# Kernel optimization log

Measured on AMD Instinct MI355X. Metric: run time of the kernel, lower is better.

Reference implementation:

```python
import jax, jax.numpy as jnp
import numpy as np

N_NODES = 100000
N_EDGES = 400000
D = 128
BN_EPS = 1e-5


def setup_inputs() -> dict:
    key = jax.random.key(0)
    ks = jax.random.split(key, 8)
    lim = 1.0 / np.sqrt(D)  # torch Linear default init range
    feature = jax.random.normal(ks[0], (N_NODES, D), dtype=jnp.float32)
    edge_index = jax.random.randint(ks[1], (2, N_EDGES), 0, N_NODES, dtype=jnp.int64)
    w1 = jax.random.uniform(ks[2], (D, D), jnp.float32, -lim, lim)
    b1 = jax.random.uniform(ks[3], (D,), jnp.float32, -lim, lim)
    w2 = jax.random.uniform(ks[4], (D, D), jnp.float32, -lim, lim)
    b2 = jax.random.uniform(ks[5], (D,), jnp.float32, -lim, lim)
    gamma = jnp.ones((D,), jnp.float32)
    beta = jnp.zeros((D,), jnp.float32)
    return {"feature": feature, "edge_index": edge_index, "w1": w1, "b1": b1,
            "w2": w2, "b2": b2, "gamma": gamma, "beta": beta}


def reference(feature, edge_index, w1, b1, w2, b2, gamma, beta):
    n = feature.shape[0]
    src, dst = edge_index[0], edge_index[1]
    # GIN aggregation (eps=0): h_i = x_i + sum_{j: (j->i)} x_j
    agg = jax.ops.segment_sum(feature[src], dst, num_segments=n)
    h = feature + agg
    # 2-layer MLP: Linear -> ReLU -> Linear (torch Linear: x @ W.T + b)
    h = jnp.maximum(h @ w1.T + b1, 0.0) @ w2.T + b2
    # ReLU then BatchNorm1d (training mode: batch stats, biased variance)
    h = jnp.maximum(h, 0.0)
    mean = jnp.mean(h, axis=0)
    var = jnp.mean(jnp.square(h - mean), axis=0)
    return (h - mean) * jax.lax.rsqrt(var + BN_EPS) * gamma + beta
```

## Files before the change

kernel.cpp:

```cpp
#include <hip/hip_runtime.h>
#include <hip/hip_bf16.h>

#define DD 128
#define TM 64
#define LD 136
#define SB 128
#define GRID_MLP 1024

typedef short bf16x8 __attribute__((ext_vector_type(8)));
typedef float f32x4  __attribute__((ext_vector_type(4)));

__device__ __forceinline__ unsigned short f2bf(float f) {
  unsigned int u = __float_as_uint(f);
  u += 0x7FFFu + ((u >> 16) & 1u);
  return (unsigned short)(u >> 16);
}
__device__ __forceinline__ unsigned int pack2(float lo, float hi) {
  return (unsigned int)f2bf(lo) | ((unsigned int)f2bf(hi) << 16);
}
__device__ __forceinline__ float bf2f(unsigned short u) {
  union { unsigned int i; float f; } x; x.i = ((unsigned int)u) << 16; return x.f;
}
__device__ __forceinline__ void add2(float* a, unsigned int w) {
  union { unsigned int i; float f; } lo, hi;
  lo.i = w << 16; hi.i = w & 0xFFFF0000u;
  a[0] += lo.f; a[1] += hi.f;
}

__global__ __launch_bounds__(256) void k_init(const float* __restrict__ w1,
                                              const float* __restrict__ w2,
                                              const float* __restrict__ feat,
                                              unsigned short* __restrict__ wbf1,
                                              unsigned short* __restrict__ wbf2,
                                              unsigned short* __restrict__ featbf,
                                              int* __restrict__ cnt, int nrows) {
  int i0 = blockIdx.x * 256 + threadIdx.x;
  int GT = gridDim.x * 256;
  for (int i = i0; i < nrows; i += GT) cnt[i] = 0;
  for (int i = i0; i < DD * DD; i += GT) { wbf1[i] = f2bf(w1[i]); wbf2[i] = f2bf(w2[i]); }
  int total8 = nrows * 16;
  for (int i = i0; i < total8; i += GT) {
    const float* fp = feat + (long long)i * 8;
    float4 a = *reinterpret_cast<const float4*>(fp);
    float4 b = *reinterpret_cast<const float4*>(fp + 4);
    uint4 u;
    u.x = pack2(a.x, a.y); u.y = pack2(a.z, a.w);
    u.z = pack2(b.x, b.y); u.w = pack2(b.z, b.w);
    *reinterpret_cast<uint4*>(featbf + (long long)i * 8) = u;
  }
}

__global__ __launch_bounds__(256) void k_hist(const int* __restrict__ ei, int* __restrict__ cnt,
                                              int ne) {
  int e = blockIdx.x * 256 + threadIdx.x;
  if (e < ne) atomicAdd(&cnt[ei[ne + e]], 1);
}

__global__ __launch_bounds__(256) void k_scan1(const int* __restrict__ cnt,
                                               int* __restrict__ bsum, int n) {
  __shared__ int red[256];
  int b = blockIdx.x, t = threadIdx.x;
  int chunk = (n + SB - 1) / SB;
  int lo = b * chunk, hi = min(n, lo + chunk);
  int s = 0;
  for (int i = lo + t; i < hi; i += 256) s += cnt[i];
  red[t] = s;
  __syncthreads();
  for (int off = 128; off; off >>= 1) {
    if (t < off) red[t] += red[t + off];
    __syncthreads();
  }
  if (t == 0) bsum[b] = red[0];
}

__global__ __launch_bounds__(256) void k_scan3(const int* __restrict__ cnt,
                                               const int* __restrict__ bsum,
                                               int* __restrict__ ofs, int* __restrict__ cur,
                                               int n) {
  __shared__ int red[256];
  __shared__ int sbs[SB];
  int b = blockIdx.x, t = threadIdx.x;

  int ov = (t < SB) ? bsum[t] : 0;
  if (t < SB) sbs[t] = ov;
  __syncthreads();
  for (int off = 1; off < SB; off <<= 1) {
    int v = (t < SB && t >= off) ? sbs[t - off] : 0;
    __syncthreads();
    if (t < SB) sbs[t] += v;
    __syncthreads();
  }
  if (t < SB) sbs[t] -= ov;
  __syncthreads();
  int base = sbs[b];
  if (b == SB - 1 && t == SB - 1) ofs[n] = sbs[t] + ov;

  int chunk  = (n + SB - 1) / SB;
  int tchunk = (chunk + 255) / 256;
  int blo = b * chunk, bhi = min(n, blo + chunk);
  int lo = blo + t * tchunk, hi = min(bhi, lo + tchunk);
  int s = 0;
  for (int i = lo; i < hi; ++i) s += cnt[i];
  int mine = s;
  red[t] = s;
  __syncthreads();
  for (int off = 1; off < 256; off <<= 1) {
    int v = (t >= off) ? red[t - off] : 0;
    __syncthreads();
    red[t] += v;
    __syncthreads();
  }
  int run = base + red[t] - mine;
  for (int i = lo; i < hi; ++i) {
    int c = cnt[i];
    ofs[i] = run; cur[i] = run;
    run += c;
  }
}

__global__ __launch_bounds__(256) void k_fill(const int* __restrict__ ei, int* __restrict__ cur,
                                              int* __restrict__ csr, int ne) {
  int e = blockIdx.x * 256 + threadIdx.x;
  if (e >= ne) return;
  int pos = atomicAdd(&cur[ei[ne + e]], 1);
  csr[pos] = ei[e];
}

__global__ __launch_bounds__(256) void k_agg(
    const unsigned short* __restrict__ featbf, const int* __restrict__ ofs,
    const int* __restrict__ csr, unsigned short* __restrict__ agg, int nrows)
{
  int t = blockIdx.x * 256 + threadIdx.x;
  int row = t >> 4;
  if (row >= nrows) return;
  int c = (t & 15) * 8;

  float a[8];
  {
    uint4 u = *reinterpret_cast<const uint4*>(featbf + (long long)row * DD + c);
    union { unsigned int i; float f; } x;
    x.i = u.x << 16; a[0] = x.f;  x.i = u.x & 0xFFFF0000u; a[1] = x.f;
    x.i = u.y << 16; a[2] = x.f;  x.i = u.y & 0xFFFF0000u; a[3] = x.f;
    x.i = u.z << 16; a[4] = x.f;  x.i = u.z & 0xFFFF0000u; a[5] = x.f;
    x.i = u.w << 16; a[6] = x.f;  x.i = u.w & 0xFFFF0000u; a[7] = x.f;
  }

  int o0 = ofs[row], o1 = ofs[row + 1];
  int j = o0;
  for (; j + 4 <= o1; j += 4) {
    uint4 u0 = *reinterpret_cast<const uint4*>(featbf + (long long)csr[j]     * DD + c);
    uint4 u1 = *reinterpret_cast<const uint4*>(featbf + (long long)csr[j + 1] * DD + c);
    uint4 u2 = *reinterpret_cast<const uint4*>(featbf + (long long)csr[j + 2] * DD + c);
    uint4 u3 = *reinterpret_cast<const uint4*>(featbf + (long long)csr[j + 3] * DD + c);
    add2(a + 0, u0.x); add2(a + 2, u0.y); add2(a + 4, u0.z); add2(a + 6, u0.w);
    add2(a + 0, u1.x); add2(a + 2, u1.y); add2(a + 4, u1.z); add2(a + 6, u1.w);
    add2(a + 0, u2.x); add2(a + 2, u2.y); add2(a + 4, u2.z); add2(a + 6, u2.w);
    add2(a + 0, u3.x); add2(a + 2, u3.y); add2(a + 4, u3.z); add2(a + 6, u3.w);
  }
  for (; j < o1; ++j) {
    uint4 u0 = *reinterpret_cast<const uint4*>(featbf + (long long)csr[j] * DD + c);
    add2(a + 0, u0.x); add2(a + 2, u0.y); add2(a + 4, u0.z); add2(a + 6, u0.w);
  }

  uint4 u;
  u.x = pack2(a[0], a[1]); u.y = pack2(a[2], a[3]);
  u.z = pack2(a[4], a[5]); u.w = pack2(a[6], a[7]);
  *reinterpret_cast<uint4*>(agg + (long long)row * DD + c) = u;
}

__global__ __launch_bounds__(256) void k_mlp(
    unsigned short* hb,
    const unsigned short* __restrict__ wbf1, const float* __restrict__ b1,
    const unsigned short* __restrict__ wbf2, const float* __restrict__ b2,
    float* __restrict__ partial, int nrows, int ntiles)
{
  __shared__ unsigned short ldsP[TM * LD];
  __shared__ unsigned short ldsH2[TM * LD];
  const int tid  = threadIdx.x;
  const int wave = tid >> 6, lane = tid & 63;
  const int q = lane >> 4, l16 = lane & 15;
  const int col0 = wave * 32;

  bf16x8 bw1[2][4], bw2[2][4];
  float bias1[2], bias2[2];
  for (int n = 0; n < 2; ++n) {
    int jc = col0 + n * 16 + l16;
    bias1[n] = b1[jc];
    bias2[n] = b2[jc];
    for (int kk = 0; kk < 4; ++kk) {
      bw1[n][kk] = *reinterpret_cast<const bf16x8*>(wbf1 + jc * DD + kk * 32 + q * 8);
      bw2[n][kk] = *reinterpret_cast<const bf16x8*>(wbf2 + jc * DD + kk * 32 + q * 8);
    }
  }

  const bf16x8 zf = {0, 0, 0, 0, 0, 0, 0, 0};
  float fs[2] = {0.f, 0.f}, fs2[2] = {0.f, 0.f};

  for (int tile = blockIdx.x; tile < ntiles; tile += GRID_MLP) {
    const int row0 = tile * TM;

    f32x4 acc[4][2];
    const f32x4 zero = {0.f, 0.f, 0.f, 0.f};
    for (int m = 0; m < 4; ++m) for (int n = 0; n < 2; ++n) acc[m][n] = zero;

    #pragma unroll
    for (int kk = 0; kk < 4; ++kk) {
      bf16x8 aF[4];
      #pragma unroll
      for (int m = 0; m < 4; ++m) {
        int row = row0 + m * 16 + l16;
        aF[m] = (row < nrows)
            ? *reinterpret_cast<const bf16x8*>(hb + (long long)row * DD + kk * 32 + q * 8)
            : zf;
      }
      #pragma unroll
      for (int m = 0; m < 4; ++m)
        #pragma unroll
        for (int n = 0; n < 2; ++n)
          acc[m][n] = __builtin_amdgcn_mfma_f32_16x16x32_bf16(aF[m], bw1[n][kk], acc[m][n], 0, 0, 0);
    }

    for (int m = 0; m < 4; ++m)
      for (int n = 0; n < 2; ++n)
        for (int r = 0; r < 4; ++r) {
          float v = fmaxf(acc[m][n][r] + bias1[n], 0.f);
          ldsH2[(m * 16 + q * 4 + r) * LD + (col0 + n * 16 + l16)] = f2bf(v);
        }
    __syncthreads();

    for (int m = 0; m < 4; ++m) for (int n = 0; n < 2; ++n) acc[m][n] = zero;

    #pragma unroll
    for (int kk = 0; kk < 4; ++kk) {
      bf16x8 aF[4];
      #pragma unroll
      for (int m = 0; m < 4; ++m)
        aF[m] = *reinterpret_cast<const bf16x8*>(&ldsH2[(m * 16 + l16) * LD + kk * 32 + q * 8]);
      #pragma unroll
      for (int m = 0; m < 4; ++m)
        #pragma unroll
        for (int n = 0; n < 2; ++n)
          acc[m][n] = __builtin_amdgcn_mfma_f32_16x16x32_bf16(aF[m], bw2[n][kk], acc[m][n], 0, 0, 0);
    }

    for (int m = 0; m < 4; ++m)
      for (int n = 0; n < 2; ++n) {
        int col = col0 + n * 16 + l16;
        for (int r = 0; r < 4; ++r) {
          int rl = m * 16 + q * 4 + r;
          float v = fmaxf(acc[m][n][r] + bias2[n], 0.f);
          ldsP[rl * LD + col] = f2bf(v);
          if (row0 + rl < nrows) { fs[n] += v; fs2[n] += v * v; }
        }
      }
    __syncthreads();

    for (int it = 0; it < 4; ++it) {
      int idx = it * 2048 + tid * 8;
      int r = idx >> 7, c = idx & 127;
      int row = row0 + r;
      if (row < nrows)
        *reinterpret_cast<uint4*>(hb + (long long)row * DD + c) =
            *reinterpret_cast<const uint4*>(&ldsP[r * LD + c]);
    }
  }

  for (int off = 16; off < 64; off <<= 1)
    for (int n = 0; n < 2; ++n) {
      fs[n]  += __shfl_xor(fs[n], off);
      fs2[n] += __shfl_xor(fs2[n], off);
    }
  if (q == 0) {
    float* pb = partial + (long long)blockIdx.x * 256;
    for (int n = 0; n < 2; ++n) {
      int col = col0 + n * 16 + l16;
      pb[col]       = fs[n];
      pb[128 + col] = fs2[n];
    }
  }
}

__global__ __launch_bounds__(256) void k_stats(const float* __restrict__ partial,
                                               const float* __restrict__ gamma,
                                               const float* __restrict__ beta,
                                               float* __restrict__ scsh, int nrows) {
  __shared__ float s0[256], s1[256];
  int c = blockIdx.x;
  int t = threadIdx.x;
  float a = 0.f, b = 0.f;
  for (int r = t; r < GRID_MLP; r += 256) {
    a += partial[(long long)r * 256 + c];
    b += partial[(long long)r * 256 + 128 + c];
  }
  s0[t] = a; s1[t] = b;
  __syncthreads();
  for (int off = 128; off; off >>= 1) {
    if (t < off) { s0[t] += s0[t + off]; s1[t] += s1[t + off]; }
    __syncthreads();
  }
  if (t == 0) {
    float mean = s0[0] / (float)nrows;
    float var  = fmaxf(s1[0] / (float)nrows - mean * mean, 0.f);
    float inv  = rsqrtf(var + 1e-5f);
    float sc   = gamma[c] * inv;
    scsh[c]       = sc;
    scsh[128 + c] = beta[c] - mean * sc;
  }
}

__global__ __launch_bounds__(256) void k_bn(const unsigned short* __restrict__ hbuf,
                                            float* __restrict__ out,
                                            const float* __restrict__ scsh,
                                            long long total8) {
  long long t = (long long)blockIdx.x * 256 + threadIdx.x;
  if (t >= total8) return;
  int c0 = (int)((t * 8) & 127);
  float4 sa = *reinterpret_cast<const float4*>(scsh + c0);
  float4 sb = *reinterpret_cast<const float4*>(scsh + c0 + 4);
  float4 ha = *reinterpret_cast<const float4*>(scsh + 128 + c0);
  float4 hb = *reinterpret_cast<const float4*>(scsh + 132 + c0);
  uint4 u = *reinterpret_cast<const uint4*>(hbuf + t * 8);
  float4 a, b;
  a.x = bf2f((unsigned short)(u.x & 0xFFFF)) * sa.x + ha.x;
  a.y = bf2f((unsigned short)(u.x >> 16))    * sa.y + ha.y;
  a.z = bf2f((unsigned short)(u.y & 0xFFFF)) * sa.z + ha.z;
  a.w = bf2f((unsigned short)(u.y >> 16))    * sa.w + ha.w;
  b.x = bf2f((unsigned short)(u.z & 0xFFFF)) * sb.x + hb.x;
  b.y = bf2f((unsigned short)(u.z >> 16))    * sb.y + hb.y;
  b.z = bf2f((unsigned short)(u.w & 0xFFFF)) * sb.z + hb.z;
  b.w = bf2f((unsigned short)(u.w >> 16))    * sb.w + hb.w;
  float* of = out + t * 8;
  *reinterpret_cast<float4*>(of)     = a;
  *reinterpret_cast<float4*>(of + 4) = b;
}

extern "C" void kernel_launch(void* const* d_in, const int* in_sizes, int n_in,
                              void* d_out, int out_size, void* d_ws, size_t ws_size,
                              hipStream_t stream) {
  const float* feat  = (const float*)d_in[0];
  const int*   eidx  = (const int*)d_in[1];
  const float* w1    = (const float*)d_in[2];
  const float* b1    = (const float*)d_in[3];
  const float* w2    = (const float*)d_in[4];
  const float* b2    = (const float*)d_in[5];
  const float* gamma = (const float*)d_in[6];
  const float* beta  = (const float*)d_in[7];
  float* out = (float*)d_out;

  const int nrows  = in_sizes[0] / DD;
  const int ne     = in_sizes[1] / 2;
  const int ntiles = (nrows + TM - 1) / TM;

  int* base = (int*)d_ws;
  unsigned short* wbf1 = (unsigned short*)base;
  unsigned short* wbf2 = (unsigned short*)(base + 8192);
  float* scsh  = (float*)(base + 16384);
  int*   ofs   = base + 16384 + 256;
  int*   cur   = ofs + (nrows + 1);
  int*   csr   = cur + nrows;
  int*   bsum  = csr + ne;
  float* partial = (float*)(bsum + SB);
  int*   cnt   = (int*)(partial + (size_t)GRID_MLP * 256);
  long long w_off = (long long)(cnt + nrows - base);
  w_off = (w_off + 3) & ~3LL;
  unsigned short* featbf = (unsigned short*)(base + w_off);
  unsigned short* hbuf   = featbf + (long long)nrows * DD;

  const long long total8 = (long long)nrows * DD / 8;
  const int agg_blocks  = (nrows * 16 + 255) / 256;

  k_init <<<2048,                         256, 0, stream>>>(w1, w2, feat, wbf1, wbf2,
                                                            featbf, cnt, nrows);
  k_hist <<<(ne + 255) / 256,             256, 0, stream>>>(eidx, cnt, ne);
  k_scan1<<<SB,                           256, 0, stream>>>(cnt, bsum, nrows);
  k_scan3<<<SB,                           256, 0, stream>>>(cnt, bsum, ofs, cur, nrows);
  k_fill <<<(ne + 255) / 256,             256, 0, stream>>>(eidx, cur, csr, ne);
  k_agg  <<<agg_blocks,                   256, 0, stream>>>(featbf, ofs, csr, hbuf, nrows);
  k_mlp  <<<GRID_MLP,                     256, 0, stream>>>(hbuf, wbf1, b1, wbf2, b2,
                                                            partial, nrows, ntiles);
  k_stats<<<128,                          256, 0, stream>>>(partial, gamma, beta, scsh, nrows);
  k_bn   <<<(int)((total8 + 255) / 256),  256, 0, stream>>>(hbuf, out, scsh, total8);
}
```

Before: 230.4 us.

## Merge scan kernels and transpose MFMA operands for packed LDS stores

Two scan kernels become one. Each block now recomputes its prefix base by summing every count before its chunk, which removes a launch and the block-sum buffer but adds redundant reads of the count array. In the MLP, the MFMA operands are swapped so each lane holds four consecutive columns of one row. Bias-ReLU results are then packed into 8-byte LDS stores instead of scattered 2-byte stores, and the BN statistic accumulation and reduction are reorganised to match.

```diff
diff --git a/kernel.cpp b/kernel.cpp
--- a/kernel.cpp
+++ b/kernel.cpp
@@ -56,50 +56,31 @@
   if (e < ne) atomicAdd(&cnt[ei[ne + e]], 1);
 }
 
-__global__ __launch_bounds__(256) void k_scan1(const int* __restrict__ cnt,
-                                               int* __restrict__ bsum, int n) {
+__global__ __launch_bounds__(256) void k_scan(const int* __restrict__ cnt,
+                                              int* __restrict__ ofs, int* __restrict__ cur,
+                                              int n) {
   __shared__ int red[256];
+  __shared__ int sbase;
   int b = blockIdx.x, t = threadIdx.x;
   int chunk = (n + SB - 1) / SB;
-  int lo = b * chunk, hi = min(n, lo + chunk);
+  int blo = b * chunk, bhi = min(n, blo + chunk);
+
   int s = 0;
-  for (int i = lo + t; i < hi; i += 256) s += cnt[i];
+  for (int i = t; i < blo; i += 256) s += cnt[i];
   red[t] = s;
   __syncthreads();
   for (int off = 128; off; off >>= 1) {
     if (t < off) red[t] += red[t + off];
     __syncthreads();
   }
-  if (t == 0) bsum[b] = red[0];
-}
-
-__global__ __launch_bounds__(256) void k_scan3(const int* __restrict__ cnt,
-                                               const int* __restrict__ bsum,
-                                               int* __restrict__ ofs, int* __restrict__ cur,
-                                               int n) {
-  __shared__ int red[256];
-  __shared__ int sbs[SB];
-  int b = blockIdx.x, t = threadIdx.x;
-
-  int ov = (t < SB) ? bsum[t] : 0;
-  if (t < SB) sbs[t] = ov;
-  __syncthreads();
-  for (int off = 1; off < SB; off <<= 1) {
-    int v = (t < SB && t >= off) ? sbs[t - off] : 0;
-    __syncthreads();
-    if (t < SB) sbs[t] += v;
-    __syncthreads();
-  }
-  if (t < SB) sbs[t] -= ov;
-  __syncthreads();
-  int base = sbs[b];
-  if (b == SB - 1 && t == SB - 1) ofs[n] = sbs[t] + ov;
-
-  int chunk  = (n + SB - 1) / SB;
+  if (t == 0) sbase = red[0];
+  __syncthreads();
+  int base = sbase;
+  __syncthreads();
+
   int tchunk = (chunk + 255) / 256;
-  int blo = b * chunk, bhi = min(n, blo + chunk);
   int lo = blo + t * tchunk, hi = min(bhi, lo + tchunk);
-  int s = 0;
+  s = 0;
   for (int i = lo; i < hi; ++i) s += cnt[i];
   int mine = s;
   red[t] = s;
@@ -116,6 +97,7 @@
     ofs[i] = run; cur[i] = run;
     run += c;
   }
+  if (b == SB - 1 && t == 255) ofs[n] = base + red[255];
 }
 
 __global__ __launch_bounds__(256) void k_fill(const int* __restrict__ ei, int* __restrict__ cur,
@@ -182,19 +164,24 @@
   const int col0 = wave * 32;
 
   bf16x8 bw1[2][4], bw2[2][4];
-  float bias1[2], bias2[2];
   for (int n = 0; n < 2; ++n) {
     int jc = col0 + n * 16 + l16;
-    bias1[n] = b1[jc];
-    bias2[n] = b2[jc];
     for (int kk = 0; kk < 4; ++kk) {
       bw1[n][kk] = *reinterpret_cast<const bf16x8*>(wbf1 + jc * DD + kk * 32 + q * 8);
       bw2[n][kk] = *reinterpret_cast<const bf16x8*>(wbf2 + jc * DD + kk * 32 + q * 8);
     }
   }
+  float bias1v[2][4], bias2v[2][4];
+  for (int n = 0; n < 2; ++n)
+    for (int r = 0; r < 4; ++r) {
+      int jc = col0 + n * 16 + q * 4 + r;
+      bias1v[n][r] = b1[jc];
+      bias2v[n][r] = b2[jc];
+    }
 
   const bf16x8 zf = {0, 0, 0, 0, 0, 0, 0, 0};
-  float fs[2] = {0.f, 0.f}, fs2[2] = {0.f, 0.f};
+  float fs[2][4] = {{0.f,0.f,0.f,0.f},{0.f,0.f,0.f,0.f}};
+  float fs2[2][4] = {{0.f,0.f,0.f,0.f},{0.f,0.f,0.f,0.f}};
 
   for (int tile = blockIdx.x; tile < ntiles; tile += GRID_MLP) {
     const int row0 = tile * TM;
@@ -217,15 +204,22 @@
       for (int m = 0; m < 4; ++m)
         #pragma unroll
         for (int n = 0; n < 2; ++n)
-          acc[m][n] = __builtin_amdgcn_mfma_f32_16x16x32_bf16(aF[m], bw1[n][kk], acc[m][n], 0, 0, 0);
-    }
-
+          acc[m][n] = __builtin_amdgcn_mfma_f32_16x16x32_bf16(bw1[n][kk], aF[m], acc[m][n], 0, 0, 0);
+    }
+
+    #pragma unroll
     for (int m = 0; m < 4; ++m)
-      for (int n = 0; n < 2; ++n)
-        for (int r = 0; r < 4; ++r) {
-          float v = fmaxf(acc[m][n][r] + bias1[n], 0.f);
-          ldsH2[(m * 16 + q * 4 + r) * LD + (col0 + n * 16 + l16)] = f2bf(v);
-        }
+      #pragma unroll
+      for (int n = 0; n < 2; ++n) {
+        float v0 = fmaxf(acc[m][n][0] + bias1v[n][0], 0.f);
+        float v1 = fmaxf(acc[m][n][1] + bias1v[n][1], 0.f);
+        float v2 = fmaxf(acc[m][n][2] + bias1v[n][2], 0.f);
+        float v3 = fmaxf(acc[m][n][3] + bias1v[n][3], 0.f);
+        uint2 w;
+        w.x = pack2(v0, v1);
+        w.y = pack2(v2, v3);
+        *reinterpret_cast<uint2*>(&ldsH2[(m * 16 + l16) * LD + col0 + n * 16 + q * 4]) = w;
+      }
     __syncthreads();
 
     for (int m = 0; m < 4; ++m) for (int n = 0; n < 2; ++n) acc[m][n] = zero;
@@ -240,19 +234,30 @@
       for (int m = 0; m < 4; ++m)
         #pragma unroll
         for (int n = 0; n < 2; ++n)
-          acc[m][n] = __builtin_amdgcn_mfma_f32_16x16x32_bf16(aF[m], bw2[n][kk], acc[m][n], 0, 0, 0);
-    }
-
-    for (int m = 0; m < 4; ++m)
+          acc[m][n] = __builtin_amdgcn_mfma_f32_16x16x32_bf16(bw2[n][kk], aF[m], acc[m][n], 0, 0, 0);
+    }
+
+    #pragma unroll
+    for (int m = 0; m < 4; ++m) {
+      bool rowok = (row0 + m * 16 + l16) < nrows;
+      #pragma unroll
       for (int n = 0; n < 2; ++n) {
-        int col = col0 + n * 16 + l16;
-        for (int r = 0; r < 4; ++r) {
-          int rl = m * 16 + q * 4 + r;
-          float v = fmaxf(acc[m][n][r] + bias2[n], 0.f);
-          ldsP[rl * LD + col] = f2bf(v);
-          if (row0 + rl < nrows) { fs[n] += v; fs2[n] += v * v; }
+        float v0 = fmaxf(acc[m][n][0] + bias2v[n][0], 0.f);
+        float v1 = fmaxf(acc[m][n][1] + bias2v[n][1], 0.f);
+        float v2 = fmaxf(acc[m][n][2] + bias2v[n][2], 0.f);
+        float v3 = fmaxf(acc[m][n][3] + bias2v[n][3], 0.f);
+        if (rowok) {
+          fs[n][0] += v0; fs2[n][0] += v0 * v0;
+          fs[n][1] += v1; fs2[n][1] += v1 * v1;
+          fs[n][2] += v2; fs2[n][2] += v2 * v2;
+          fs[n][3] += v3; fs2[n][3] += v3 * v3;
         }
-      }
+        uint2 w;
+        w.x = pack2(v0, v1);
+        w.y = pack2(v2, v3);
+        *reinterpret_cast<uint2*>(&ldsP[(m * 16 + l16) * LD + col0 + n * 16 + q * 4]) = w;
+      }
+    }
     __syncthreads();
 
     for (int it = 0; it < 4; ++it) {
@@ -265,18 +270,20 @@
     }
   }
 
-  for (int off = 16; off < 64; off <<= 1)
-    for (int n = 0; n < 2; ++n) {
-      fs[n]  += __shfl_xor(fs[n], off);
-      fs2[n] += __shfl_xor(fs2[n], off);
-    }
-  if (q == 0) {
+  for (int off = 1; off < 16; off <<= 1)
+    for (int n = 0; n < 2; ++n)
+      for (int r = 0; r < 4; ++r) {
+        fs[n][r]  += __shfl_xor(fs[n][r], off);
+        fs2[n][r] += __shfl_xor(fs2[n][r], off);
+      }
+  if (l16 == 0) {
     float* pb = partial + (long long)blockIdx.x * 256;
-    for (int n = 0; n < 2; ++n) {
-      int col = col0 + n * 16 + l16;
-      pb[col]       = fs[n];
-      pb[128 + col] = fs2[n];
-    }
+    for (int n = 0; n < 2; ++n)
+      for (int r = 0; r < 4; ++r) {
+        int col = col0 + n * 16 + q * 4 + r;
+        pb[col]       = fs[n][r];
+        pb[128 + col] = fs2[n][r];
+      }
   }
 }
 
@@ -358,8 +365,7 @@
   int*   ofs   = base + 16384 + 256;
   int*   cur   = ofs + (nrows + 1);
   int*   csr   = cur + nrows;
-  int*   bsum  = csr + ne;
-  float* partial = (float*)(bsum + SB);
+  float* partial = (float*)(csr + ne);
   int*   cnt   = (int*)(partial + (size_t)GRID_MLP * 256);
   long long w_off = (long long)(cnt + nrows - base);
   w_off = (w_off + 3) & ~3LL;
@@ -372,8 +378,7 @@
   k_init <<<2048,                         256, 0, stream>>>(w1, w2, feat, wbf1, wbf2,
                                                             featbf, cnt, nrows);
   k_hist <<<(ne + 255) / 256,             256, 0, stream>>>(eidx, cnt, ne);
-  k_scan1<<<SB,                           256, 0, stream>>>(cnt, bsum, nrows);
-  k_scan3<<<SB,                           256, 0, stream>>>(cnt, bsum, ofs, cur, nrows);
+  k_scan <<<SB,                           256, 0, stream>>>(cnt, ofs, cur, nrows);
   k_fill <<<(ne + 255) / 256,             256, 0, stream>>>(eidx, cur, csr, ne);
   k_agg  <<<agg_blocks,                   256, 0, stream>>>(featbf, ofs, csr, hbuf, nrows);
   k_mlp  <<<GRID_MLP,                     256, 0, stream>>>(hbuf, wbf1, b1, wbf2, b2,
```

After: 280.3 us. 21.6% more time.
